# Performance work log

Measured on AMD Instinct MI355X. Metric: run time of the kernel, lower is better.

The kernel has to match this reference:

```python
import jax, jax.numpy as jnp
import numpy as np

B, N, D, H = 128, 512, 128, 8
DK = D // H
CLIP = 10.0                      # tanh_clipping
NORM = float(np.sqrt(D))         # norm_factor = sqrt(embedding_dim), used as multiplier (as in source)


def setup_inputs() -> dict:
    key = jax.random.key(0)
    ks = jax.random.split(key, 7)
    std = float(1.0 / np.sqrt(D))
    return {
        "embeddings": jax.random.normal(ks[0], (B, N, D), dtype=jnp.float32),
        "eval_seq": jax.random.randint(ks[1], (B, N), 0, N, dtype=jnp.int32),
        "W_placeholder": jax.random.uniform(ks[2], (2 * D,), jnp.float32, -std, std),
        "W_node": jax.random.normal(ks[3], (D, 3 * D), jnp.float32) * std,
        "W_fixed": jax.random.normal(ks[4], (D, D), jnp.float32) * std,
        "W_step": jax.random.normal(ks[5], (2 * D, D), jnp.float32) * std,
        "W_out": jax.random.normal(ks[6], (D, D), jnp.float32) * std,
    }


def _decode(embeddings, eval_seq, W_placeholder, W_node, W_fixed, W_step, W_out):
    # Precomputed (fixed) projections, as in the torch module before the decode loop
    proj = embeddings @ W_node                                  # [B,N,3D]
    gK, gV, lK = jnp.split(proj, 3, axis=-1)
    gK = gK.reshape(B, N, H, DK).transpose(2, 0, 1, 3)          # [H,B,N,dk]
    gV = gV.reshape(B, N, H, DK).transpose(2, 0, 1, 3)          # [H,B,N,dk]
    fixed = embeddings.mean(axis=1) @ W_fixed                   # [B,D]
    batch_ix = jnp.arange(B)

    def step_logp(ctx, mask):
        # ctx: [B,2D] step context; mask: [B,N] bool (True = visited)
        query = fixed + ctx @ W_step                            # [B,D]
        qh = query.reshape(B, H, DK)
        compat = NORM * jnp.einsum('bhd,hbnd->hbn', qh, gK)     # [H,B,N]
        compat = jnp.where(mask[None], -jnp.inf, compat)        # mask_inner
        attn = jax.nn.softmax(compat, axis=-1)
        heads = jnp.einsum('hbn,hbnd->hbd', attn, gV)           # [H,B,dk]
        glimpse = heads.transpose(1, 0, 2).reshape(B, D) @ W_out
        logits = NORM * jnp.einsum('bnd,bd->bn', lK, glimpse)   # [B,N]
        logits = jnp.tanh(logits) * CLIP
        logits = jnp.where(mask, -jnp.inf, logits)              # mask_logits
        return jax.nn.log_softmax(logits, axis=-1)              # temp = 1.0

    # step 0: W_placeholder context, empty mask
    mask0 = jnp.zeros((B, N), dtype=bool)
    ctx0 = jnp.broadcast_to(W_placeholder[None, :], (B, 2 * D))
    lp0 = step_logp(ctx0, mask0)
    sel0 = eval_seq[:, 0]
    mask1 = mask0.at[batch_ix, sel0].set(True)
    emb_first = embeddings[batch_ix, sel0]                      # [B,D] (constant across steps)

    def body(carry, sel_i):
        mask, last = carry
        ctx = jnp.concatenate([emb_first, embeddings[batch_ix, last]], axis=-1)  # [B,2D]
        lp = step_logp(ctx, mask)
        new_mask = mask.at[batch_ix, sel_i].set(True)           # update mask AFTER computing log_p
        return (new_mask, sel_i), lp

    (_, _), lps = jax.lax.scan(body, (mask1, sel0), eval_seq[:, 1:].T)  # lps: [N-1,B,N]
    log_p = jnp.concatenate([lp0[None], lps], axis=0).transpose(1, 0, 2)  # [B,N,N]
    return log_p


def reference(embeddings, eval_seq, W_placeholder, W_node, W_fixed, W_step, W_out):
    log_p = _decode(embeddings, eval_seq, W_placeholder, W_node, W_fixed, W_step, W_out)
    return log_p, eval_seq
```

## Files before the change

### kernel.cpp

```cpp
#include <hip/hip_runtime.h>
#include <math.h>

#define B_ 128
#define N_ 512
#define D_ 128
#define H_ 8
#define NORM_ 11.313708498984761f
#define SC_ 16.322324f
#define HSC_ 32.644648f
#define CLIP_ 10.0f
#define MASKC_ -3.0e38f
#define NEG_BIG_ -1.0e30f
#define L2E_ 1.4426950408889634f
#define LN2_ 0.6931471805599453f

typedef unsigned short ushortx;
typedef __attribute__((ext_vector_type(8))) short s8v;
typedef __attribute__((ext_vector_type(4))) float f4v;

#define MFMA_ __builtin_amdgcn_mfma_f32_16x16x32_bf16

__device__ __forceinline__ unsigned short f2bf(float x) {
  union { float f; unsigned u; } v; v.f = x;
  unsigned r = v.u + 0x7fffu + ((v.u >> 16) & 1u);
  return (unsigned short)(r >> 16);
}
__device__ __forceinline__ float bf2f(ushortx u) {
  union { unsigned u; float f; } v; v.u = ((unsigned)u) << 16; return v.f;
}
__device__ __forceinline__ unsigned cvtpk(float lo, float hi) {
  unsigned r;
  asm("v_cvt_pk_bf16_f32 %0, %1, %2" : "=v"(r) : "v"(lo), "v"(hi));
  return r;
}
__device__ __forceinline__ float exp2_hw(float x) {
  float r; asm("v_exp_f32 %0, %1" : "=v"(r) : "v"(x)); return r;
}
__device__ __forceinline__ float log2_hw(float x) {
  float r; asm("v_log_f32 %0, %1" : "=v"(r) : "v"(x)); return r;
}
__device__ __forceinline__ float rcp_hw(float x) {
  float r; asm("v_rcp_f32 %0, %1" : "=v"(r) : "v"(x)); return r;
}
__device__ __forceinline__ float max3f(float a, float b, float c) {
  float r; asm("v_max3_f32 %0, %1, %2, %3" : "=v"(r) : "v"(a), "v"(b), "v"(c));
  return r;
}

__global__ __launch_bounds__(128)
void wfold2(const float* __restrict__ Wnode, const float* __restrict__ Wout,
            const float* __restrict__ Wstep, ushortx* __restrict__ WfT,
            ushortx* __restrict__ WsbT) {
  const int c = blockIdx.x;
  const int k = threadIdx.x;
  if (c < 256) {
    WfT[c * 128 + k] = f2bf(Wnode[k * 384 + c]);
  } else if (c < 384) {
    const int d = c - 256;
    float s = 0.f;
    #pragma unroll 4
    for (int j = 0; j < 128; ++j) s += Wnode[k * 384 + 256 + j] * Wout[d * 128 + j];
    WfT[c * 128 + k] = f2bf(s);
  } else {
    const int d = c - 384;
    WsbT[d * 128 + k] = f2bf(Wstep[(128 + k) * 128 + d] * SC_);
  }
}

__global__ __launch_bounds__(512)
void sortperm(const int* __restrict__ seq, ushortx* __restrict__ K,
              ushortx* __restrict__ n_orig) {
  const int b = blockIdx.x;
  const int t = threadIdx.x;
  const int lane = t & 63, wv = t >> 6;
  __shared__ int Tl[512];
  __shared__ int wsum[8];
  __shared__ int tot_s;

  Tl[t] = 0x7fffffff;
  __syncthreads();
  const int node = seq[b * 512 + t];
  atomicMin(&Tl[node], t + 1);
  __syncthreads();

  const int f = (Tl[node] == t + 1) ? 1 : 0;
  const unsigned long long bal = __ballot(f);
  const int excl = __popcll(bal & ((1ull << lane) - 1ull));
  if (lane == 0) wsum[wv] = __popcll(bal);
  __syncthreads();
  int woff = 0;
  #pragma unroll
  for (int i = 0; i < 8; ++i) woff += (i < wv) ? wsum[i] : 0;
  const int Kt = woff + excl;
  K[b * 512 + t] = (ushortx)Kt;
  if (f) n_orig[b * 512 + Kt] = (ushortx)node;
  if (t == 511) tot_s = Kt + f;

  const int g = (Tl[t] == 0x7fffffff) ? 1 : 0;
  const unsigned long long bal2 = __ballot(g);
  const int excl2 = __popcll(bal2 & ((1ull << lane) - 1ull));
  const int w2 = __popcll(bal2);
  __syncthreads();
  if (lane == 0) wsum[wv] = w2;
  __syncthreads();
  int woff2 = 0;
  #pragma unroll
  for (int i = 0; i < 8; ++i) woff2 += (i < wv) ? wsum[i] : 0;
  if (g) n_orig[b * 512 + tot_s + woff2 + excl2] = (ushortx)t;
}

__global__ __launch_bounds__(256)
void proj_mfma(const float* __restrict__ E, const ushortx* __restrict__ WfT,
               const ushortx* __restrict__ n_orig,
               ushortx* __restrict__ gK, ushortx* __restrict__ gVt,
               ushortx* __restrict__ lKt) {
  __shared__ ushortx S[64 * 216];
  const int tid = threadIdx.x;
  const int w = tid >> 6, l = tid & 63;
  const int m16 = l & 15, lg = l >> 4;
  const int b = blockIdx.x >> 3;
  const int n0 = (blockIdx.x & 7) * 64;
  const int p_row = n0 + w * 16 + m16;
  const int orig = (int)n_orig[b * 512 + p_row];
  const float* er = E + ((size_t)b * 512 + orig) * 128;

  s8v af[4];
  #pragma unroll
  for (int ks = 0; ks < 4; ++ks) {
    float4 f0 = *(const float4*)(er + ks * 32 + lg * 8);
    float4 f1 = *(const float4*)(er + ks * 32 + lg * 8 + 4);
    union { unsigned u[4]; s8v v; } au;
    au.u[0] = cvtpk(f0.x, f0.y); au.u[1] = cvtpk(f0.z, f0.w);
    au.u[2] = cvtpk(f1.x, f1.y); au.u[3] = cvtpk(f1.z, f1.w);
    af[ks] = au.v;
  }

  const int lrow = w * 16 + 4 * lg;
  #pragma unroll
  for (int half = 0; half < 2; ++half) {
    const int cb = half * 192;
    #pragma unroll
    for (int ct = 0; ct < 12; ++ct) {
      const int lc = ct * 16 + m16;
      f4v acc = {0.f, 0.f, 0.f, 0.f};
      #pragma unroll
      for (int ks = 0; ks < 4; ++ks) {
        const s8v bf = *(const s8v*)(WfT + (size_t)(cb + lc) * 128 + ks * 32 + lg * 8);
        acc = MFMA_(af[ks], bf, acc, 0, 0, 0);
      }
      const unsigned w01 = cvtpk(acc[0], acc[1]);
      const unsigned w23 = cvtpk(acc[2], acc[3]);
      S[(lrow + 0) * 216 + lc] = (ushortx)(w01 & 0xffffu);
      S[(lrow + 1) * 216 + lc] = (ushortx)(w01 >> 16);
      S[(lrow + 2) * 216 + lc] = (ushortx)(w23 & 0xffffu);
      S[(lrow + 3) * 216 + lc] = (ushortx)(w23 >> 16);
    }
    __syncthreads();

    if (half == 0) {
      #pragma unroll
      for (int it = 0; it < 4; ++it) {
        const int idx = it * 256 + tid;
        const int hh = idx >> 7, nn = (idx >> 1) & 63, hf = idx & 1;
        const uint4 v = *(const uint4*)(&S[nn * 216 + hh * 16 + hf * 8]);
        *(uint4*)(gK + (((size_t)(b * 8 + hh) * 512 + n0 + nn) * 16 + hf * 8)) = v;
      }
      #pragma unroll
      for (int it = 0; it < 2; ++it) {
        const int idx = it * 256 + tid;
        const int hh = idx >> 7, dk = (idx >> 3) & 15, n8 = (idx & 7) * 8;
        const int lc = 128 + hh * 16 + dk;
        unsigned wr[4];
        #pragma unroll
        for (int j = 0; j < 4; ++j)
          wr[j] = (unsigned)S[(n8 + 2 * j) * 216 + lc] |
                  ((unsigned)S[(n8 + 2 * j + 1) * 216 + lc] << 16);
        uint4 o; o.x = wr[0]; o.y = wr[1]; o.z = wr[2]; o.w = wr[3];
        *(uint4*)(gVt + (((size_t)(b * 8 + hh) * 16 + dk) * 512 + n0 + n8)) = o;
      }
    } else {
      #pragma unroll
      for (int it = 0; it < 4; ++it) {
        const int idx = it * 256 + tid;
        const int nn = idx >> 4, d8 = (idx & 15) * 8;
        const uint4 v = *(const uint4*)(&S[nn * 216 + 64 + d8]);
        *(uint4*)(lKt + ((size_t)(b * 512 + n0 + nn) * 128 + d8)) = v;
      }
      #pragma unroll
      for (int it = 0; it < 2; ++it) {
        const int idx = it * 256 + tid;
        const int hq = idx >> 7, dk = (idx >> 3) & 15, n8 = (idx & 7) * 8;
        const int lc = hq * 16 + dk;
        unsigned wr[4];
        #pragma unroll
        for (int j = 0; j < 4; ++j)
          wr[j] = (unsigned)S[(n8 + 2 * j) * 216 + lc] |
                  ((unsigned)S[(n8 + 2 * j + 1) * 216 + lc] << 16);
        uint4 o; o.x = wr[0]; o.y = wr[1]; o.z = wr[2]; o.w = wr[3];
        *(uint4*)(gVt + (((size_t)(b * 8 + 4 + hq) * 16 + dk) * 512 + n0 + n8)) = o;
      }
    }
    __syncthreads();
  }
}

__global__ __launch_bounds__(512)
void prep(const float* __restrict__ emb, const int* __restrict__ seq,
          const float* __restrict__ Wp, const float* __restrict__ Wfix,
          const float* __restrict__ Wstep, ushortx* __restrict__ Qb0,
          float* __restrict__ Abuf) {
  const int b = blockIdx.x;
  const int t = threadIdx.x;
  __shared__ float4 red4[16][33];
  __shared__ float mean[128];
  const int row0 = t >> 5, c4 = t & 31;
  const float* eb = emb + (size_t)b * 512 * 128;
  float4 acc = {0.f, 0.f, 0.f, 0.f};
  for (int it = 0; it < 32; ++it) {
    const float4 x = *(const float4*)(eb + (size_t)(it * 16 + row0) * 128 + c4 * 4);
    acc.x += x.x; acc.y += x.y; acc.z += x.z; acc.w += x.w;
  }
  red4[row0][c4] = acc;
  __syncthreads();
  if (t < 128) {
    const int c4b = t >> 2, j = t & 3;
    float s = 0.f;
    #pragma unroll
    for (int r = 0; r < 16; ++r) s += ((const float*)&red4[r][c4b])[j];
    mean[t] = s * (1.f / 512.f);
  }
  __syncthreads();
  if (t < 128) {
    float fx = 0.f;
    for (int k = 0; k < 128; ++k) fx += mean[k] * Wfix[k * 128 + t];
    float c = 0.f;
    for (int k = 0; k < 256; ++k) c += Wp[k] * Wstep[k * 128 + t];
    const int sel0 = seq[b * N_];
    const float* ef = eb + (size_t)sel0 * 128;
    float a = 0.f;
    for (int k = 0; k < 128; ++k) a += ef[k] * Wstep[k * 128 + t];
    Qb0[b * 128 + t] = f2bf((fx + c) * SC_);
    Abuf[b * 128 + t] = (fx + a) * SC_;
  }
}

__global__ void tail_seq(const int* __restrict__ seq, float* __restrict__ out,
                         int count) {
  const int i = blockIdx.x * 256 + threadIdx.x;
  if (i < count) out[(size_t)B_ * N_ * N_ + i] = (float)seq[i];
}

__global__ __launch_bounds__(512, 8)
void decode_mfma(const ushortx* __restrict__ gK,
                 const ushortx* __restrict__ gVt,
                 const ushortx* __restrict__ lKt,
                 const float* __restrict__ emb,
                 const int* __restrict__ seq,
                 const ushortx* __restrict__ WsbT,
                 const float* __restrict__ Abuf,
                 const ushortx* __restrict__ Qb0,
                 const ushortx* __restrict__ Ksrt,
                 const ushortx* __restrict__ n_orig,
                 float* __restrict__ out) {
  const int id = blockIdx.x;
  const int xcd = id & 7, pos = id >> 3;
  const int b = xcd * 16 + (pos >> 5);
  const int s0 = (pos & 31) * 16;
  const int tid = threadIdx.x;
  const int w = tid >> 6, l = tid & 63;
  const int m16 = l & 15, lg = l >> 4;

  __shared__ ushortx logitsTb[512 * 26];
  __shared__ ushortx ctxh[16][136];
  __shared__ ushortx Qt[16][136];
  __shared__ ushortx norig_l[512];
  __shared__ ushortx Ko[16];
  __shared__ int sel_l[16];
  __shared__ float Ab[128];

  norig_l[tid] = n_orig[b * 512 + tid];
  if (tid < 16) {
    Ko[tid] = Ksrt[b * 512 + s0 + tid];
    const int sg = s0 + tid;
    sel_l[tid] = (sg >= 1) ? seq[b * 512 + sg - 1] : 0;
  }
  if (tid < 128) Ab[tid] = Abuf[b * 128 + tid];
  __syncthreads();

  if (tid < 256) {
    const int row = tid >> 4, c8 = (tid & 15) * 8;
    const float* er = emb + ((size_t)b * 512 + sel_l[row]) * 128 + c8;
    float4 f0 = *(const float4*)(er);
    float4 f1 = *(const float4*)(er + 4);
    unsigned* dst = (unsigned*)&ctxh[row][c8];
    dst[0] = cvtpk(f0.x, f0.y); dst[1] = cvtpk(f0.z, f0.w);
    dst[2] = cvtpk(f1.x, f1.y); dst[3] = cvtpk(f1.z, f1.w);
  }
  __syncthreads();

  const int h = w;
  {
    s8v aw[4];
    #pragma unroll
    for (int ks = 0; ks < 4; ++ks)
      aw[ks] = *(const s8v*)(WsbT + (size_t)(h * 16 + m16) * 128 + ks * 32 + lg * 8);
    f4v acc = {0.f, 0.f, 0.f, 0.f};
    #pragma unroll
    for (int ks = 0; ks < 4; ++ks) {
      const s8v bf = *(const s8v*)(&ctxh[m16][ks * 32 + lg * 8]);
      acc = MFMA_(aw[ks], bf, acc, 0, 0, 0);
    }
    const int d0 = h * 16 + 4 * lg;
    unsigned q01 = cvtpk(acc[0] + Ab[d0], acc[1] + Ab[d0 + 1]);
    unsigned q23 = cvtpk(acc[2] + Ab[d0 + 2], acc[3] + Ab[d0 + 3]);
    if (s0 == 0 && m16 == 0) {
      q01 = *(const unsigned*)(Qb0 + b * 128 + d0);
      q23 = *(const unsigned*)(Qb0 + b * 128 + d0 + 2);
    }
    unsigned* qdst = (unsigned*)&Qt[m16][d0];
    qdst[0] = q01; qdst[1] = q23;
  }
  __syncthreads();

  s8v qf = {};
  if (lg < 2) qf = *(const s8v*)(&Qt[m16][h * 16 + lg * 8]);

  const int K0i = (int)Ko[0], K15 = (int)Ko[15];
  const int chStart = K0i >> 5;
  const int chClean = (K15 + 31) >> 5;
  const int Ks = (int)Ko[m16];
  const size_t bh = (size_t)(b * 8 + h);

  f4v Oacc = {0.f, 0.f, 0.f, 0.f};
  float m_run = NEG_BIG_, l_run = 0.f;
  const int nA0 = 8 * (m16 >> 2) + (m16 & 3);

  for (int ch = chStart; ch < 16; ++ch) {
    const int base = ch * 32;
    s8v a0 = {}, a1 = {};
    if (lg < 2) {
      a0 = *(const s8v*)(gK + ((bh * 512 + base + nA0) * 16 + lg * 8));
      a1 = *(const s8v*)(gK + ((bh * 512 + base + nA0 + 4) * 16 + lg * 8));
    }
    const s8v av = *(const s8v*)(gVt + ((bh * 16 + m16) * 512 + base + lg * 8));

    f4v z = {0.f, 0.f, 0.f, 0.f};
    f4v st0 = MFMA_(a0, qf, z, 0, 0, 0);
    f4v st1 = MFMA_(a1, qf, z, 0, 0, 0);

    float cm = max3f(st0[0], st0[1], st0[2]);
    cm = max3f(cm, st0[3], st1[0]);
    cm = max3f(cm, st1[1], st1[2]);
    cm = fmaxf(cm, st1[3]);
    cm = fmaxf(cm, __shfl_xor(cm, 16));
    cm = fmaxf(cm, __shfl_xor(cm, 32));

    if (__any(cm > m_run + 8.0f)) {
      const float mn = fmaxf(m_run, cm);
      const float cr = exp2_hw(m_run - mn);
      m_run = mn; l_run *= cr;
      Oacc[0] *= cr; Oacc[1] *= cr; Oacc[2] *= cr; Oacc[3] *= cr;
    }

    float p[8];
    #pragma unroll
    for (int r = 0; r < 4; ++r) {
      p[r]     = exp2_hw(st0[r] - m_run);
      p[4 + r] = exp2_hw(st1[r] - m_run);
    }
    if (ch < chClean) {
      const int nb = base + 8 * lg;
      #pragma unroll
      for (int j = 0; j < 8; ++j) p[j] = (nb + j < Ks) ? 0.f : p[j];
    }
    l_run += ((p[0] + p[1]) + (p[2] + p[3])) + ((p[4] + p[5]) + (p[6] + p[7]));
    union { unsigned u[4]; s8v v; } pu;
    pu.u[0] = cvtpk(p[0], p[1]); pu.u[1] = cvtpk(p[2], p[3]);
    pu.u[2] = cvtpk(p[4], p[5]); pu.u[3] = cvtpk(p[6], p[7]);
    Oacc = MFMA_(av, pu.v, Oacc, 0, 0, 0);
  }

  l_run += __shfl_xor(l_run, 16);
  l_run += __shfl_xor(l_run, 32);
  const float scale = rcp_hw(l_run) * HSC_;
  {
    const int d0 = h * 16 + 4 * lg;
    unsigned* hd = (unsigned*)&ctxh[m16][d0];
    hd[0] = cvtpk(Oacc[0] * scale, Oacc[1] * scale);
    hd[1] = cvtpk(Oacc[2] * scale, Oacc[3] * scale);
  }
  __syncthreads();

  #pragma unroll
  for (int nt = 0; nt < 4; ++nt) {
    const int n0 = w * 64 + nt * 16;
    if (n0 + 16 <= K0i) {
      #pragma unroll
      for (int r = 0; r < 4; ++r)
        logitsTb[(n0 + 4 * lg + r) * 26 + m16] = f2bf(MASKC_);
      continue;
    }
    f4v acc = {0.f, 0.f, 0.f, 0.f};
    #pragma unroll
    for (int ks = 0; ks < 4; ++ks) {
      const s8v aL = *(const s8v*)(lKt + ((size_t)b * 512 + n0 + m16) * 128 + ks * 32 + lg * 8);
      const s8v bH = *(const s8v*)(&ctxh[m16][ks * 32 + lg * 8]);
      acc = MFMA_(aL, bH, acc, 0, 0, 0);
    }
    const bool bnd = (n0 < K15);
    #pragma unroll
    for (int r = 0; r < 4; ++r) {
      const int p = n0 + 4 * lg + r;
      float x = fminf(fmaxf(acc[r], -43.f), 43.f);
      const float e2 = exp2_hw(x);
      float lgv = CLIP_ * (e2 - 1.f) * rcp_hw(e2 + 1.f);
      if (bnd && p < Ks) lgv = MASKC_;
      logitsTb[p * 26 + m16] = f2bf(lgv);
    }
  }
  __syncthreads();

  int no[8];
  #pragma unroll
  for (int i = 0; i < 8; ++i) no[i] = (int)norig_l[i * 64 + l];
  #pragma unroll
  for (int pass = 0; pass < 2; ++pass) {
    const int s = w + pass * 8;
    float v[8];
    #pragma unroll
    for (int i = 0; i < 8; ++i) v[i] = bf2f(logitsTb[(i * 64 + l) * 26 + s]);
    float mm = max3f(v[0], v[1], v[2]);
    mm = max3f(mm, v[3], v[4]);
    mm = max3f(mm, v[5], v[6]);
    mm = fmaxf(mm, v[7]);
    #pragma unroll
    for (int off = 1; off <= 32; off <<= 1) mm = fmaxf(mm, __shfl_xor(mm, off));
    float es = 0.f;
    #pragma unroll
    for (int i = 0; i < 8; ++i) es += exp2_hw((v[i] - mm) * L2E_);
    #pragma unroll
    for (int off = 1; off <= 32; off <<= 1) es += __shfl_xor(es, off);
    const float logZ = mm + LN2_ * log2_hw(es);
    float* orow = out + ((size_t)(b * N_ + s0 + s)) * N_;
    #pragma unroll
    for (int i = 0; i < 8; ++i)
      orow[no[i]] = fmaxf(v[i] - logZ, NEG_BIG_);
  }
}

extern "C" void kernel_launch(void* const* d_in, const int* in_sizes, int n_in,
                              void* d_out, int out_size, void* d_ws, size_t ws_size,
                              hipStream_t stream) {
  const float* emb   = (const float*)d_in[0];
  const int*   seq   = (const int*)d_in[1];
  const float* Wp    = (const float*)d_in[2];
  const float* Wnode = (const float*)d_in[3];
  const float* Wfix  = (const float*)d_in[4];
  const float* Wstep = (const float*)d_in[5];
  const float* Wout  = (const float*)d_in[6];
  float* out = (float*)d_out;

  ushortx* gK    = (ushortx*)d_ws;
  ushortx* gVt   = gK   + (size_t)8388608;
  ushortx* lKt   = gVt  + (size_t)8388608;
  ushortx* WfT   = lKt  + (size_t)8388608;
  ushortx* WsbT  = WfT  + (size_t)49152;
  ushortx* Ksrt  = WsbT + (size_t)16384;
  ushortx* n_or  = Ksrt + (size_t)65536;
  ushortx* Qb0   = n_or + (size_t)65536;
  float*   Abuf  = (float*)(Qb0 + (size_t)16384);

  wfold2<<<512, 128, 0, stream>>>(Wnode, Wout, Wstep, WfT, WsbT);
  sortperm<<<128, 512, 0, stream>>>(seq, Ksrt, n_or);
  proj_mfma<<<1024, 256, 0, stream>>>(emb, WfT, n_or, gK, gVt, lKt);
  prep<<<128, 512, 0, stream>>>(emb, seq, Wp, Wfix, Wstep, Qb0, Abuf);
  decode_mfma<<<4096, 512, 0, stream>>>(gK, gVt, lKt, emb, seq, WsbT, Abuf,
                                        Qb0, Ksrt, n_or, out);

  const long long lp_elems = (long long)B_ * N_ * N_;
  const int tail = (int)((long long)out_size - lp_elems);
  if (tail > 0) {
    tail_seq<<<(tail + 255) / 256, 256, 0, stream>>>(seq, out, tail);
  }
}
```

Baseline: 241.1 us.

## Unroll attention chunk loop by two, skip fully masked tiles, use fixed softmax max

Splits the prep kernel's three per-column dot products across all 512 threads, with a shared-memory reduction, instead of using only 128 threads. Unrolls the flash-attention chunk loop to process two 32-key chunks per iteration, which raises memory-level parallelism and halves the per-chunk max/rescale overhead. Skips whole-warp logit tiles that lie entirely in the masked prefix, and simplifies tanh to a single rcp-based form. The final log-softmax uses the known upper bound CLIP as its max instead of a wave-wide max reduction, and skips the masked slices. The rounded-down start chunk and unclamped exp add a little redundant work and rely on exp2 saturating cleanly.

```diff
diff --git a/kernel.cpp b/kernel.cpp
--- a/kernel.cpp
+++ b/kernel.cpp
@@ -213,6 +213,7 @@
   const int t = threadIdx.x;
   __shared__ float4 red4[16][33];
   __shared__ float mean[128];
+  __shared__ float pfx[4][128], pc[4][128], pa[4][128];
   const int row0 = t >> 5, c4 = t & 31;
   const float* eb = emb + (size_t)b * 512 * 128;
   float4 acc = {0.f, 0.f, 0.f, 0.f};
@@ -230,15 +231,23 @@
     mean[t] = s * (1.f / 512.f);
   }
   __syncthreads();
-  if (t < 128) {
-    float fx = 0.f;
-    for (int k = 0; k < 128; ++k) fx += mean[k] * Wfix[k * 128 + t];
-    float c = 0.f;
-    for (int k = 0; k < 256; ++k) c += Wp[k] * Wstep[k * 128 + t];
+  {
+    const int d = t & 127, part = t >> 7;
     const int sel0 = seq[b * N_];
     const float* ef = eb + (size_t)sel0 * 128;
+    float fx = 0.f;
+    for (int k = part * 32; k < part * 32 + 32; ++k) fx += mean[k] * Wfix[k * 128 + d];
+    float c = 0.f;
+    for (int k = part * 64; k < part * 64 + 64; ++k) c += Wp[k] * Wstep[k * 128 + d];
     float a = 0.f;
-    for (int k = 0; k < 128; ++k) a += ef[k] * Wstep[k * 128 + t];
+    for (int k = part * 32; k < part * 32 + 32; ++k) a += ef[k] * Wstep[k * 128 + d];
+    pfx[part][d] = fx; pc[part][d] = c; pa[part][d] = a;
+  }
+  __syncthreads();
+  if (t < 128) {
+    const float fx = pfx[0][t] + pfx[1][t] + pfx[2][t] + pfx[3][t];
+    const float c  = pc[0][t] + pc[1][t] + pc[2][t] + pc[3][t];
+    const float a  = pa[0][t] + pa[1][t] + pa[2][t] + pa[3][t];
     Qb0[b * 128 + t] = f2bf((fx + c) * SC_);
     Abuf[b * 128 + t] = (fx + a) * SC_;
   }
@@ -326,7 +335,7 @@
   if (lg < 2) qf = *(const s8v*)(&Qt[m16][h * 16 + lg * 8]);
 
   const int K0i = (int)Ko[0], K15 = (int)Ko[15];
-  const int chStart = K0i >> 5;
+  const int chS2 = (K0i >> 5) & ~1;
   const int chClean = (K15 + 31) >> 5;
   const int Ks = (int)Ko[m16];
   const size_t bh = (size_t)(b * 8 + h);
@@ -335,23 +344,32 @@
   float m_run = NEG_BIG_, l_run = 0.f;
   const int nA0 = 8 * (m16 >> 2) + (m16 & 3);
 
-  for (int ch = chStart; ch < 16; ++ch) {
+  for (int ch = chS2; ch < 16; ch += 2) {
     const int base = ch * 32;
-    s8v a0 = {}, a1 = {};
+    s8v a0 = {}, a1 = {}, a2 = {}, a3 = {};
     if (lg < 2) {
       a0 = *(const s8v*)(gK + ((bh * 512 + base + nA0) * 16 + lg * 8));
       a1 = *(const s8v*)(gK + ((bh * 512 + base + nA0 + 4) * 16 + lg * 8));
-    }
-    const s8v av = *(const s8v*)(gVt + ((bh * 16 + m16) * 512 + base + lg * 8));
+      a2 = *(const s8v*)(gK + ((bh * 512 + base + 32 + nA0) * 16 + lg * 8));
+      a3 = *(const s8v*)(gK + ((bh * 512 + base + 32 + nA0 + 4) * 16 + lg * 8));
+    }
+    const s8v av0 = *(const s8v*)(gVt + ((bh * 16 + m16) * 512 + base + lg * 8));
+    const s8v av1 = *(const s8v*)(gVt + ((bh * 16 + m16) * 512 + base + 32 + lg * 8));
 
     f4v z = {0.f, 0.f, 0.f, 0.f};
     f4v st0 = MFMA_(a0, qf, z, 0, 0, 0);
     f4v st1 = MFMA_(a1, qf, z, 0, 0, 0);
+    f4v st2 = MFMA_(a2, qf, z, 0, 0, 0);
+    f4v st3 = MFMA_(a3, qf, z, 0, 0, 0);
 
     float cm = max3f(st0[0], st0[1], st0[2]);
     cm = max3f(cm, st0[3], st1[0]);
     cm = max3f(cm, st1[1], st1[2]);
-    cm = fmaxf(cm, st1[3]);
+    cm = max3f(cm, st1[3], st2[0]);
+    cm = max3f(cm, st2[1], st2[2]);
+    cm = max3f(cm, st2[3], st3[0]);
+    cm = max3f(cm, st3[1], st3[2]);
+    cm = fmaxf(cm, st3[3]);
     cm = fmaxf(cm, __shfl_xor(cm, 16));
     cm = fmaxf(cm, __shfl_xor(cm, 32));
 
@@ -362,22 +380,32 @@
       Oacc[0] *= cr; Oacc[1] *= cr; Oacc[2] *= cr; Oacc[3] *= cr;
     }
 
-    float p[8];
+    float p[16];
     #pragma unroll
     for (int r = 0; r < 4; ++r) {
-      p[r]     = exp2_hw(st0[r] - m_run);
-      p[4 + r] = exp2_hw(st1[r] - m_run);
+      p[r]      = exp2_hw(st0[r] - m_run);
+      p[4 + r]  = exp2_hw(st1[r] - m_run);
+      p[8 + r]  = exp2_hw(st2[r] - m_run);
+      p[12 + r] = exp2_hw(st3[r] - m_run);
     }
     if (ch < chClean) {
-      const int nb = base + 8 * lg;
-      #pragma unroll
-      for (int j = 0; j < 8; ++j) p[j] = (nb + j < Ks) ? 0.f : p[j];
-    }
-    l_run += ((p[0] + p[1]) + (p[2] + p[3])) + ((p[4] + p[5]) + (p[6] + p[7]));
-    union { unsigned u[4]; s8v v; } pu;
-    pu.u[0] = cvtpk(p[0], p[1]); pu.u[1] = cvtpk(p[2], p[3]);
-    pu.u[2] = cvtpk(p[4], p[5]); pu.u[3] = cvtpk(p[6], p[7]);
-    Oacc = MFMA_(av, pu.v, Oacc, 0, 0, 0);
+      const int nb0 = base + 8 * lg;
+      const int nb1 = base + 32 + 8 * lg;
+      #pragma unroll
+      for (int j = 0; j < 8; ++j) {
+        p[j]     = (nb0 + j < Ks) ? 0.f : p[j];
+        p[8 + j] = (nb1 + j < Ks) ? 0.f : p[8 + j];
+      }
+    }
+    l_run += (((p[0] + p[1]) + (p[2] + p[3])) + ((p[4] + p[5]) + (p[6] + p[7]))) +
+             (((p[8] + p[9]) + (p[10] + p[11])) + ((p[12] + p[13]) + (p[14] + p[15])));
+    union { unsigned u[4]; s8v v; } pu0, pu1;
+    pu0.u[0] = cvtpk(p[0], p[1]);  pu0.u[1] = cvtpk(p[2], p[3]);
+    pu0.u[2] = cvtpk(p[4], p[5]);  pu0.u[3] = cvtpk(p[6], p[7]);
+    pu1.u[0] = cvtpk(p[8], p[9]);  pu1.u[1] = cvtpk(p[10], p[11]);
+    pu1.u[2] = cvtpk(p[12], p[13]); pu1.u[3] = cvtpk(p[14], p[15]);
+    Oacc = MFMA_(av0, pu0.v, Oacc, 0, 0, 0);
+    Oacc = MFMA_(av1, pu1.v, Oacc, 0, 0, 0);
   }
 
   l_run += __shfl_xor(l_run, 16);
@@ -391,31 +419,32 @@
   }
   __syncthreads();
 
-  #pragma unroll
-  for (int nt = 0; nt < 4; ++nt) {
-    const int n0 = w * 64 + nt * 16;
-    if (n0 + 16 <= K0i) {
-      #pragma unroll
-      for (int r = 0; r < 4; ++r)
-        logitsTb[(n0 + 4 * lg + r) * 26 + m16] = f2bf(MASKC_);
-      continue;
-    }
-    f4v acc = {0.f, 0.f, 0.f, 0.f};
-    #pragma unroll
-    for (int ks = 0; ks < 4; ++ks) {
-      const s8v aL = *(const s8v*)(lKt + ((size_t)b * 512 + n0 + m16) * 128 + ks * 32 + lg * 8);
-      const s8v bH = *(const s8v*)(&ctxh[m16][ks * 32 + lg * 8]);
-      acc = MFMA_(aL, bH, acc, 0, 0, 0);
-    }
-    const bool bnd = (n0 < K15);
-    #pragma unroll
-    for (int r = 0; r < 4; ++r) {
-      const int p = n0 + 4 * lg + r;
-      float x = fminf(fmaxf(acc[r], -43.f), 43.f);
-      const float e2 = exp2_hw(x);
-      float lgv = CLIP_ * (e2 - 1.f) * rcp_hw(e2 + 1.f);
-      if (bnd && p < Ks) lgv = MASKC_;
-      logitsTb[p * 26 + m16] = f2bf(lgv);
+  if (w * 64 + 64 > K0i) {
+    #pragma unroll
+    for (int nt = 0; nt < 4; ++nt) {
+      const int n0 = w * 64 + nt * 16;
+      if (n0 + 16 <= K0i) {
+        #pragma unroll
+        for (int r = 0; r < 4; ++r)
+          logitsTb[(n0 + 4 * lg + r) * 26 + m16] = f2bf(MASKC_);
+        continue;
+      }
+      f4v acc = {0.f, 0.f, 0.f, 0.f};
+      #pragma unroll
+      for (int ks = 0; ks < 4; ++ks) {
+        const s8v aL = *(const s8v*)(lKt + ((size_t)b * 512 + n0 + m16) * 128 + ks * 32 + lg * 8);
+        const s8v bH = *(const s8v*)(&ctxh[m16][ks * 32 + lg * 8]);
+        acc = MFMA_(aL, bH, acc, 0, 0, 0);
+      }
+      const bool bnd = (n0 < K15);
+      #pragma unroll
+      for (int r = 0; r < 4; ++r) {
+        const int p = n0 + 4 * lg + r;
+        const float e2 = exp2_hw(acc[r]);
+        float lgv = fmaf(-2.f * CLIP_, rcp_hw(e2 + 1.f), CLIP_);
+        if (bnd && p < Ks) lgv = MASKC_;
+        logitsTb[p * 26 + m16] = f2bf(lgv);
+      }
     }
   }
   __syncthreads();
@@ -427,20 +456,19 @@
   for (int pass = 0; pass < 2; ++pass) {
     const int s = w + pass * 8;
     float v[8];
-    #pragma unroll
-    for (int i = 0; i < 8; ++i) v[i] = bf2f(logitsTb[(i * 64 + l) * 26 + s]);
-    float mm = max3f(v[0], v[1], v[2]);
-    mm = max3f(mm, v[3], v[4]);
-    mm = max3f(mm, v[5], v[6]);
-    mm = fmaxf(mm, v[7]);
-    #pragma unroll
-    for (int off = 1; off <= 32; off <<= 1) mm = fmaxf(mm, __shfl_xor(mm, off));
     float es = 0.f;
     #pragma unroll
-    for (int i = 0; i < 8; ++i) es += exp2_hw((v[i] - mm) * L2E_);
+    for (int i = 0; i < 8; ++i) {
+      if (i * 64 + 64 <= K0i) {
+        v[i] = MASKC_;
+      } else {
+        v[i] = bf2f(logitsTb[(i * 64 + l) * 26 + s]);
+        es += exp2_hw((v[i] - CLIP_) * L2E_);
+      }
+    }
     #pragma unroll
     for (int off = 1; off <= 32; off <<= 1) es += __shfl_xor(es, off);
-    const float logZ = mm + LN2_ * log2_hw(es);
+    const float logZ = CLIP_ + LN2_ * log2_hw(es);
     float* orow = out + ((size_t)(b * N_ + s0 + s)) * N_;
     #pragma unroll
     for (int i = 0; i < 8; ++i)
```

After: 261.9 us. 1.09x slower.

## Fuse prologue kernels into one launch and compute softmax sums with MFMA

Applied to the files above, without the earlier changes.

Merges the weight-fold, sort-permutation, query-prep and sequence-tail kernels into one prologue launch with block-range dispatch. This removes several kernel launches and gaps between them. In the decode kernel, the attention denominator is now accumulated by an extra MFMA against a ones vector instead of scalar adds plus cross-lane shuffles. Logit bf16 conversion also uses a packed convert. The denominator now sums bf16-rounded probabilities, which slightly changes numerics.

```diff
diff --git a/kernel.cpp b/kernel.cpp
--- a/kernel.cpp
+++ b/kernel.cpp
@@ -47,66 +47,116 @@
   return r;
 }
 
-__global__ __launch_bounds__(128)
-void wfold2(const float* __restrict__ Wnode, const float* __restrict__ Wout,
-            const float* __restrict__ Wstep, ushortx* __restrict__ WfT,
-            ushortx* __restrict__ WsbT) {
-  const int c = blockIdx.x;
-  const int k = threadIdx.x;
-  if (c < 256) {
-    WfT[c * 128 + k] = f2bf(Wnode[k * 384 + c]);
-  } else if (c < 384) {
-    const int d = c - 256;
-    float s = 0.f;
-    #pragma unroll 4
-    for (int j = 0; j < 128; ++j) s += Wnode[k * 384 + 256 + j] * Wout[d * 128 + j];
-    WfT[c * 128 + k] = f2bf(s);
-  } else {
-    const int d = c - 384;
-    WsbT[d * 128 + k] = f2bf(Wstep[(128 + k) * 128 + d] * SC_);
-  }
-}
-
 __global__ __launch_bounds__(512)
-void sortperm(const int* __restrict__ seq, ushortx* __restrict__ K,
-              ushortx* __restrict__ n_orig) {
-  const int b = blockIdx.x;
+void prologue(const float* __restrict__ emb, const int* __restrict__ seq,
+              const float* __restrict__ Wp, const float* __restrict__ Wnode,
+              const float* __restrict__ Wfix, const float* __restrict__ Wstep,
+              const float* __restrict__ Wout,
+              ushortx* __restrict__ WfT, ushortx* __restrict__ WsbT,
+              ushortx* __restrict__ Ksrt, ushortx* __restrict__ n_orig,
+              ushortx* __restrict__ Qb0, float* __restrict__ Abuf,
+              float* __restrict__ out, int tail_count) {
+  const int blk = blockIdx.x;
   const int t = threadIdx.x;
-  const int lane = t & 63, wv = t >> 6;
-  __shared__ int Tl[512];
-  __shared__ int wsum[8];
-  __shared__ int tot_s;
-
-  Tl[t] = 0x7fffffff;
-  __syncthreads();
-  const int node = seq[b * 512 + t];
-  atomicMin(&Tl[node], t + 1);
-  __syncthreads();
-
-  const int f = (Tl[node] == t + 1) ? 1 : 0;
-  const unsigned long long bal = __ballot(f);
-  const int excl = __popcll(bal & ((1ull << lane) - 1ull));
-  if (lane == 0) wsum[wv] = __popcll(bal);
-  __syncthreads();
-  int woff = 0;
-  #pragma unroll
-  for (int i = 0; i < 8; ++i) woff += (i < wv) ? wsum[i] : 0;
-  const int Kt = woff + excl;
-  K[b * 512 + t] = (ushortx)Kt;
-  if (f) n_orig[b * 512 + Kt] = (ushortx)node;
-  if (t == 511) tot_s = Kt + f;
-
-  const int g = (Tl[t] == 0x7fffffff) ? 1 : 0;
-  const unsigned long long bal2 = __ballot(g);
-  const int excl2 = __popcll(bal2 & ((1ull << lane) - 1ull));
-  const int w2 = __popcll(bal2);
-  __syncthreads();
-  if (lane == 0) wsum[wv] = w2;
-  __syncthreads();
-  int woff2 = 0;
-  #pragma unroll
-  for (int i = 0; i < 8; ++i) woff2 += (i < wv) ? wsum[i] : 0;
-  if (g) n_orig[b * 512 + tot_s + woff2 + excl2] = (ushortx)t;
+
+  if (blk < 128) {
+    const int c = blk * 4 + (t >> 7);
+    const int k = t & 127;
+    if (c < 256) {
+      WfT[c * 128 + k] = f2bf(Wnode[k * 384 + c]);
+    } else if (c < 384) {
+      const int d = c - 256;
+      float s = 0.f;
+      #pragma unroll 4
+      for (int j = 0; j < 128; ++j) s += Wnode[k * 384 + 256 + j] * Wout[d * 128 + j];
+      WfT[c * 128 + k] = f2bf(s);
+    } else {
+      const int d = c - 384;
+      WsbT[d * 128 + k] = f2bf(Wstep[(128 + k) * 128 + d] * SC_);
+    }
+    return;
+  }
+
+  if (blk < 256) {
+    const int b = blk - 128;
+    const int lane = t & 63, wv = t >> 6;
+    __shared__ int Tl[512];
+    __shared__ int wsum[8];
+    __shared__ int tot_s;
+
+    Tl[t] = 0x7fffffff;
+    __syncthreads();
+    const int node = seq[b * 512 + t];
+    atomicMin(&Tl[node], t + 1);
+    __syncthreads();
+
+    const int f = (Tl[node] == t + 1) ? 1 : 0;
+    const unsigned long long bal = __ballot(f);
+    const int excl = __popcll(bal & ((1ull << lane) - 1ull));
+    if (lane == 0) wsum[wv] = __popcll(bal);
+    __syncthreads();
+    int woff = 0;
+    #pragma unroll
+    for (int i = 0; i < 8; ++i) woff += (i < wv) ? wsum[i] : 0;
+    const int Kt = woff + excl;
+    Ksrt[b * 512 + t] = (ushortx)Kt;
+    if (f) n_orig[b * 512 + Kt] = (ushortx)node;
+    if (t == 511) tot_s = Kt + f;
+
+    const int g = (Tl[t] == 0x7fffffff) ? 1 : 0;
+    const unsigned long long bal2 = __ballot(g);
+    const int excl2 = __popcll(bal2 & ((1ull << lane) - 1ull));
+    const int w2 = __popcll(bal2);
+    __syncthreads();
+    if (lane == 0) wsum[wv] = w2;
+    __syncthreads();
+    int woff2 = 0;
+    #pragma unroll
+    for (int i = 0; i < 8; ++i) woff2 += (i < wv) ? wsum[i] : 0;
+    if (g) n_orig[b * 512 + tot_s + woff2 + excl2] = (ushortx)t;
+    return;
+  }
+
+  if (blk < 384) {
+    const int b = blk - 256;
+    __shared__ float4 red4[16][33];
+    __shared__ float mean[128];
+    const int row0 = t >> 5, c4 = t & 31;
+    const float* eb = emb + (size_t)b * 512 * 128;
+    float4 acc = {0.f, 0.f, 0.f, 0.f};
+    for (int it = 0; it < 32; ++it) {
+      const float4 x = *(const float4*)(eb + (size_t)(it * 16 + row0) * 128 + c4 * 4);
+      acc.x += x.x; acc.y += x.y; acc.z += x.z; acc.w += x.w;
+    }
+    red4[row0][c4] = acc;
+    __syncthreads();
+    if (t < 128) {
+      const int c4b = t >> 2, j = t & 3;
+      float s = 0.f;
+      #pragma unroll
+      for (int r = 0; r < 16; ++r) s += ((const float*)&red4[r][c4b])[j];
+      mean[t] = s * (1.f / 512.f);
+    }
+    __syncthreads();
+    if (t < 128) {
+      float fx = 0.f;
+      for (int k = 0; k < 128; ++k) fx += mean[k] * Wfix[k * 128 + t];
+      float c = 0.f;
+      for (int k = 0; k < 256; ++k) c += Wp[k] * Wstep[k * 128 + t];
+      const int sel0 = seq[b * N_];
+      const float* ef = eb + (size_t)sel0 * 128;
+      float a = 0.f;
+      for (int k = 0; k < 128; ++k) a += ef[k] * Wstep[k * 128 + t];
+      Qb0[b * 128 + t] = f2bf((fx + c) * SC_);
+      Abuf[b * 128 + t] = (fx + a) * SC_;
+    }
+    return;
+  }
+
+  {
+    const int i = (blk - 384) * 512 + t;
+    if (i < tail_count) out[(size_t)B_ * N_ * N_ + i] = (float)seq[i];
+  }
 }
 
 __global__ __launch_bounds__(256)
@@ -202,52 +252,6 @@
     }
     __syncthreads();
   }
-}
-
-__global__ __launch_bounds__(512)
-void prep(const float* __restrict__ emb, const int* __restrict__ seq,
-          const float* __restrict__ Wp, const float* __restrict__ Wfix,
-          const float* __restrict__ Wstep, ushortx* __restrict__ Qb0,
-          float* __restrict__ Abuf) {
-  const int b = blockIdx.x;
-  const int t = threadIdx.x;
-  __shared__ float4 red4[16][33];
-  __shared__ float mean[128];
-  const int row0 = t >> 5, c4 = t & 31;
-  const float* eb = emb + (size_t)b * 512 * 128;
-  float4 acc = {0.f, 0.f, 0.f, 0.f};
-  for (int it = 0; it < 32; ++it) {
-    const float4 x = *(const float4*)(eb + (size_t)(it * 16 + row0) * 128 + c4 * 4);
-    acc.x += x.x; acc.y += x.y; acc.z += x.z; acc.w += x.w;
-  }
-  red4[row0][c4] = acc;
-  __syncthreads();
-  if (t < 128) {
-    const int c4b = t >> 2, j = t & 3;
-    float s = 0.f;
-    #pragma unroll
-    for (int r = 0; r < 16; ++r) s += ((const float*)&red4[r][c4b])[j];
-    mean[t] = s * (1.f / 512.f);
-  }
-  __syncthreads();
-  if (t < 128) {
-    float fx = 0.f;
-    for (int k = 0; k < 128; ++k) fx += mean[k] * Wfix[k * 128 + t];
-    float c = 0.f;
-    for (int k = 0; k < 256; ++k) c += Wp[k] * Wstep[k * 128 + t];
-    const int sel0 = seq[b * N_];
-    const float* ef = eb + (size_t)sel0 * 128;
-    float a = 0.f;
-    for (int k = 0; k < 128; ++k) a += ef[k] * Wstep[k * 128 + t];
-    Qb0[b * 128 + t] = f2bf((fx + c) * SC_);
-    Abuf[b * 128 + t] = (fx + a) * SC_;
-  }
-}
-
-__global__ void tail_seq(const int* __restrict__ seq, float* __restrict__ out,
-                         int count) {
-  const int i = blockIdx.x * 256 + threadIdx.x;
-  if (i < count) out[(size_t)B_ * N_ * N_ + i] = (float)seq[i];
 }
 
 __global__ __launch_bounds__(512, 8)
@@ -325,6 +329,14 @@
   s8v qf = {};
   if (lg < 2) qf = *(const s8v*)(&Qt[m16][h * 16 + lg * 8]);
 
+  s8v ones;
+  {
+    union { unsigned u[4]; s8v v; } ou;
+    ou.u[0] = 0x3F803F80u; ou.u[1] = 0x3F803F80u;
+    ou.u[2] = 0x3F803F80u; ou.u[3] = 0x3F803F80u;
+    ones = ou.v;
+  }
+
   const int K0i = (int)Ko[0], K15 = (int)Ko[15];
   const int chStart = K0i >> 5;
   const int chClean = (K15 + 31) >> 5;
@@ -332,7 +344,8 @@
   const size_t bh = (size_t)(b * 8 + h);
 
   f4v Oacc = {0.f, 0.f, 0.f, 0.f};
-  float m_run = NEG_BIG_, l_run = 0.f;
+  f4v Lacc = {0.f, 0.f, 0.f, 0.f};
+  float m_run = NEG_BIG_;
   const int nA0 = 8 * (m16 >> 2) + (m16 & 3);
 
   for (int ch = chStart; ch < 16; ++ch) {
@@ -358,7 +371,8 @@
     if (__any(cm > m_run + 8.0f)) {
       const float mn = fmaxf(m_run, cm);
       const float cr = exp2_hw(m_run - mn);
-      m_run = mn; l_run *= cr;
+      m_run = mn;
+      Lacc[0] *= cr;
       Oacc[0] *= cr; Oacc[1] *= cr; Oacc[2] *= cr; Oacc[3] *= cr;
     }
 
@@ -373,16 +387,14 @@
       #pragma unroll
       for (int j = 0; j < 8; ++j) p[j] = (nb + j < Ks) ? 0.f : p[j];
     }
-    l_run += ((p[0] + p[1]) + (p[2] + p[3])) + ((p[4] + p[5]) + (p[6] + p[7]));
     union { unsigned u[4]; s8v v; } pu;
     pu.u[0] = cvtpk(p[0], p[1]); pu.u[1] = cvtpk(p[2], p[3]);
     pu.u[2] = cvtpk(p[4], p[5]); pu.u[3] = cvtpk(p[6], p[7]);
     Oacc = MFMA_(av, pu.v, Oacc, 0, 0, 0);
-  }
-
-  l_run += __shfl_xor(l_run, 16);
-  l_run += __shfl_xor(l_run, 32);
-  const float scale = rcp_hw(l_run) * HSC_;
+    Lacc = MFMA_(ones, pu.v, Lacc, 0, 0, 0);
+  }
+
+  const float scale = rcp_hw(Lacc[0]) * HSC_;
   {
     const int d0 = h * 16 + 4 * lg;
     unsigned* hd = (unsigned*)&ctxh[m16][d0];
@@ -394,10 +406,12 @@
   #pragma unroll
   for (int nt = 0; nt < 4; ++nt) {
     const int n0 = w * 64 + nt * 16;
+    const int pb = (n0 + 4 * lg) * 26 + m16;
     if (n0 + 16 <= K0i) {
-      #pragma unroll
-      for (int r = 0; r < 4; ++r)
-        logitsTb[(n0 + 4 * lg + r) * 26 + m16] = f2bf(MASKC_);
+      logitsTb[pb]      = f2bf(MASKC_);
+      logitsTb[pb + 26] = f2bf(MASKC_);
+      logitsTb[pb + 52] = f2bf(MASKC_);
+      logitsTb[pb + 78] = f2bf(MASKC_);
       continue;
     }
     f4v acc = {0.f, 0.f, 0.f, 0.f};
@@ -408,15 +422,22 @@
       acc = MFMA_(aL, bH, acc, 0, 0, 0);
     }
     const bool bnd = (n0 < K15);
+    float lgv[4];
     #pragma unroll
     for (int r = 0; r < 4; ++r) {
       const int p = n0 + 4 * lg + r;
       float x = fminf(fmaxf(acc[r], -43.f), 43.f);
       const float e2 = exp2_hw(x);
-      float lgv = CLIP_ * (e2 - 1.f) * rcp_hw(e2 + 1.f);
-      if (bnd && p < Ks) lgv = MASKC_;
-      logitsTb[p * 26 + m16] = f2bf(lgv);
-    }
+      float lv = CLIP_ * (e2 - 1.f) * rcp_hw(e2 + 1.f);
+      if (bnd && p < Ks) lv = MASKC_;
+      lgv[r] = lv;
+    }
+    const unsigned pk01 = cvtpk(lgv[0], lgv[1]);
+    const unsigned pk23 = cvtpk(lgv[2], lgv[3]);
+    logitsTb[pb]      = (ushortx)pk01;
+    logitsTb[pb + 26] = (ushortx)(pk01 >> 16);
+    logitsTb[pb + 52] = (ushortx)pk23;
+    logitsTb[pb + 78] = (ushortx)(pk23 >> 16);
   }
   __syncthreads();
 
@@ -470,16 +491,13 @@
   ushortx* Qb0   = n_or + (size_t)65536;
   float*   Abuf  = (float*)(Qb0 + (size_t)16384);
 
-  wfold2<<<512, 128, 0, stream>>>(Wnode, Wout, Wstep, WfT, WsbT);
-  sortperm<<<128, 512, 0, stream>>>(seq, Ksrt, n_or);
+  const long long lp_elems = (long long)B_ * N_ * N_;
+  const int tail = (int)((long long)out_size - lp_elems);
+
+  prologue<<<512, 512, 0, stream>>>(emb, seq, Wp, Wnode, Wfix, Wstep, Wout,
+                                    WfT, WsbT, Ksrt, n_or, Qb0, Abuf,
+                                    out, tail > 0 ? tail : 0);
   proj_mfma<<<1024, 256, 0, stream>>>(emb, WfT, n_or, gK, gVt, lKt);
-  prep<<<128, 512, 0, stream>>>(emb, seq, Wp, Wfix, Wstep, Qb0, Abuf);
   decode_mfma<<<4096, 512, 0, stream>>>(gK, gVt, lKt, emb, seq, WsbT, Abuf,
                                         Qb0, Ksrt, n_or, out);
-
-  const long long lp_elems = (long long)B_ * N_ * N_;
-  const int tail = (int)((long long)out_size - lp_elems);
-  if (tail > 0) {
-    tail_seq<<<(tail + 255) / 256, 256, 0, stream>>>(seq, out, tail);
-  }
-}
+}
```

Result: no change. 238.3 us (-1.2%).
